# Kernel optimization log

Hardware: AMD Instinct MI355X
Metric: run time of the kernel (lower is better)

Reference implementation:

```python
import jax, jax.numpy as jnp
import numpy as np

N, E, G = 100000, 600000, 64  # nodes, edges, graphs
F_IN, W, EPS = 32, 128, 1e-5


def setup_inputs() -> dict:
    key = jax.random.key(0)
    ks = jax.random.split(key, 16)
    p = lambda k, shape: jax.random.normal(k, shape, dtype=jnp.float32) * 0.1
    z = lambda n: jnp.zeros((n,), jnp.float32)
    o = lambda n: jnp.ones((n,), jnp.float32)
    return {
        "x": jax.random.normal(ks[0], (N, F_IN), dtype=jnp.float32),
        "edge_index": jax.random.randint(ks[1], (2, E), 0, N, dtype=jnp.int32),
        "batch": jnp.sort(jax.random.randint(ks[2], (N,), 0, G, dtype=jnp.int32)),
        # GCNConv layers
        "W1": p(ks[3], (F_IN, W)), "b1": z(W),
        "W2": p(ks[4], (W, W)), "b2": z(W),
        # mlp_first: Linear -> BN -> ReLU -> Linear
        "W3": p(ks[5], (W, W)), "b3": z(W), "g1": o(W), "be1": z(W),
        "W4": p(ks[6], (W, W)), "b4": z(W),
        # mlp: Linear -> BN -> ReLU -> Linear
        "W5": p(ks[7], (W, W // 2)), "b5": z(W // 2), "g2": o(W // 2), "be2": z(W // 2),
        "W6": p(ks[8], (W // 2, 1)), "b6": z(1),
    }


def gcn_conv(x, src, dst, Wt, b):
    # PyG GCNConv with add_self_loops=True: D^-1/2 (A+I) D^-1/2 (x W) + b
    h = x @ Wt  # [N, width]
    deg = jax.ops.segment_sum(jnp.ones(src.shape[0], x.dtype), dst, num_segments=N) + 1.0
    dinv = jax.lax.rsqrt(deg)
    norm = dinv[src] * dinv[dst]  # per-edge normalization
    agg = jax.ops.segment_sum(h[src] * norm[:, None], dst, num_segments=N)
    # self-loop term: norm for (i,i) is 1/deg[i]
    return agg + h * (dinv * dinv)[:, None] + b


def batch_norm(x, g, b):
    # training-mode BatchNorm1d (batch stats, biased var)
    mu = x.mean(axis=0)
    var = jnp.mean((x - mu) ** 2, axis=0)
    return (x - mu) * jax.lax.rsqrt(var + EPS) * g + b


def reference(x, edge_index, batch, W1, b1, W2, b2, W3, b3, g1, be1, W4, b4, W5, b5, g2, be2, W6, b6):
    src, dst = edge_index[0], edge_index[1]
    x = jax.nn.relu(gcn_conv(x, src, dst, W1, b1))
    x = jax.nn.relu(gcn_conv(x, src, dst, W2, b2))
    # mlp_first + ReLU
    x = jax.nn.relu(batch_norm(x @ W3 + b3, g1, be1)) @ W4 + b4
    x = jax.nn.relu(x)
    # global max pool over nodes per graph
    x = jax.ops.segment_max(x, batch, num_segments=G)  # [G, width]
    # final mlp
    x = jax.nn.relu(batch_norm(x @ W5 + b5, g2, be2)) @ W6 + b6
    return x[:, 0]
```

## Files before the change

### kernel.cpp

```cpp
#include <hip/hip_runtime.h>

#define N_NODES 100000
#define N_EDGES 600000
#define N_GRAPHS 64
#define EPS 1e-5f
#define SCAN_BLOCKS 391

typedef unsigned short u16;
typedef unsigned int u32;
typedef __attribute__((ext_vector_type(8))) short bf16x8;
typedef __attribute__((ext_vector_type(4))) float f32x4;

__device__ __forceinline__ float bf2f(u16 u) { return __uint_as_float(((u32)u) << 16); }
__device__ __forceinline__ u16 f2bf(float f) {
    u32 u = __float_as_uint(f);
    u += 0x7FFFu + ((u >> 16) & 1u);
    return (u16)(u >> 16);
}
__device__ __forceinline__ float2 bfx2(u32 v) {
    float2 r;
    r.x = __uint_as_float(v << 16);
    r.y = __uint_as_float(v & 0xFFFF0000u);
    return r;
}

#define WS_COUNTS   ((size_t)0)
#define WS_CURSOR   ((size_t)400384)
#define WS_POOLED   ((size_t)800768)
#define WS_BNSUM    ((size_t)833536)
#define WS_BNSUMSQ  ((size_t)834048)
#define WS_FLAG     ((size_t)834560)
#define ZERO_BYTES  ((size_t)835072)
#define WS_OFFSETS  ((size_t)835072)
#define WS_DINV     ((size_t)1235456)
#define WS_DINV2    ((size_t)1635840)
#define WS_SRCS     ((size_t)2036224)
#define WS_ZF       ((size_t)4436736)
#define WS_CANONW   ((size_t)4453120)
#define WS_BUFA     ((size_t)4578560)
#define WS_BUFB     ((size_t)30178560)

#define CW_W1 0
#define CW_B1 4096
#define CW_W2 4224
#define CW_B2 20608
#define CW_W3 20736
#define CW_B3 37120
#define CW_G1 37248
#define CW_BE1 37376
#define CW_W4 37504
#define CW_B4 53888
#define CW_W5 54016
#define CW_B5 62208
#define CW_G2 62272
#define CW_BE2 62336
#define CW_W6 62400
#define CW_B6 62464

__global__ void detect_kernel(const u32* __restrict__ xraw, int* __restrict__ flag) {
    __shared__ int cnt;
    if (threadIdx.x == 0) cnt = 0;
    __syncthreads();
    int c = 0;
    for (int i = threadIdx.x; i < 2048; i += 256) {
        u32 w = xraw[i];
        float a = fabsf(__uint_as_float((w & 0xFFFFu) << 16));
        if (a == 0.f || (a > 1e-8f && a < 1e4f)) c++;
    }
    atomicAdd(&cnt, c);
    __syncthreads();
    if (threadIdx.x == 0) *flag = (cnt > 1024) ? 1 : 0;
}

__global__ void convx_kernel(const void* __restrict__ xsrc, u16* __restrict__ dst,
                             const int* __restrict__ flag, const float* __restrict__ dinv) {
    int i = blockIdx.x * 256 + threadIdx.x;
    if (i < N_NODES * 32) {
        float v = (*flag) ? bf2f(((const u16*)xsrc)[i]) : ((const float*)xsrc)[i];
        dst[i] = f2bf(v * dinv[i >> 5]);
    }
}

struct SmallArgs {
    const void* src[16];
    int n[16];
    int off[16];
    int cols[16];
};
__global__ void convs_kernel(SmallArgs a, u16* __restrict__ dst, const int* __restrict__ flag) {
    int i = blockIdx.x * 256 + threadIdx.x;
    int isbf = *flag;
#pragma unroll
    for (int j = 0; j < 16; j++)
        if (i < a.n[j]) {
            u16 v = isbf ? ((const u16*)a.src[j])[i] : f2bf(((const float*)a.src[j])[i]);
            if (a.cols[j] > 0) {
                int k = i / a.cols[j];
                int n = i - k * a.cols[j];
                int Kd = a.n[j] / a.cols[j];
                dst[a.off[j] + n * Kd + k] = v;
            } else {
                dst[a.off[j] + i] = v;
            }
        }
}

__global__ void deg_kernel(const int* __restrict__ dst, int* __restrict__ counts) {
    int e = blockIdx.x * 256 + threadIdx.x;
    if (e < N_EDGES) atomicAdd(&counts[dst[e]], 1);
}

__global__ __launch_bounds__(256) void reduce_kernel(const int* __restrict__ counts,
                                                     int* __restrict__ partials) {
    int i = blockIdx.x * 256 + threadIdx.x;
    int v = (i < N_NODES) ? counts[i] : 0;
    for (int off = 32; off > 0; off >>= 1) v += __shfl_down(v, off, 64);
    __shared__ int wsum[4];
    if ((threadIdx.x & 63) == 0) wsum[threadIdx.x >> 6] = v;
    __syncthreads();
    if (threadIdx.x == 0) partials[blockIdx.x] = wsum[0] + wsum[1] + wsum[2] + wsum[3];
}

__global__ __launch_bounds__(512) void scanpart_kernel(int* __restrict__ partials) {
    __shared__ int sc[512];
    int t = threadIdx.x;
    int v = (t < SCAN_BLOCKS) ? partials[t] : 0;
    sc[t] = v;
    __syncthreads();
    for (int off = 1; off < 512; off <<= 1) {
        int u = (t >= off) ? sc[t - off] : 0;
        __syncthreads();
        sc[t] += u;
        __syncthreads();
    }
    if (t < SCAN_BLOCKS) partials[t] = sc[t] - v;
}

__global__ __launch_bounds__(256) void offsets_kernel(const int* __restrict__ counts,
                                                      const int* __restrict__ partials,
                                                      int* __restrict__ offs,
                                                      float* __restrict__ dinv) {
    int i = blockIdx.x * 256 + threadIdx.x;
    int lane = threadIdx.x & 63, wv = threadIdx.x >> 6;
    int v = (i < N_NODES) ? counts[i] : 0;
    int sv = v;
    for (int off = 1; off < 64; off <<= 1) {
        int u = __shfl_up(sv, off, 64);
        if (lane >= off) sv += u;
    }
    __shared__ int wsum[4];
    if (lane == 63) wsum[wv] = sv;
    __syncthreads();
    int wpre = 0;
    for (int w = 0; w < wv; w++) wpre += wsum[w];
    int excl = sv - v + wpre + partials[blockIdx.x];
    if (i < N_NODES) {
        offs[i] = excl;
        dinv[i] = rsqrtf((float)(v + 1));
    }
    if (i == N_NODES - 1) offs[N_NODES] = excl + v;
}

__global__ void scatter_kernel(const int* __restrict__ src, const int* __restrict__ dst,
                               const int* __restrict__ offs, int* __restrict__ cursor,
                               int* __restrict__ srcs) {
    int e = blockIdx.x * 256 + threadIdx.x;
    if (e < N_EDGES) {
        int d = dst[e];
        int p = offs[d] + atomicAdd(&cursor[d], 1);
        srcs[p] = src[e];
    }
}

__global__ __launch_bounds__(256, 3) void gemmx_kernel(
    const u16* __restrict__ xs, const u16* __restrict__ W1t, const u16* __restrict__ b1,
    const u16* __restrict__ W2t, u16* __restrict__ C, const float* __restrict__ dinv,
    const int* __restrict__ goffs, const int* __restrict__ gsrcs, int M) {
    __shared__ __align__(16) u16 ldsA[128 * 40];
    __shared__ __align__(16) u16 ldsB[128 * 136];

    const int tid = threadIdx.x;
    const int wave = tid >> 6;
    const int lane = tid & 63;
    const int l15 = lane & 15;
    const int quad = lane >> 4;
    const int row0 = blockIdx.x * 128 + wave * 32;

    {
        const u32* g = (const u32*)W1t;
        u32* l = (u32*)ldsA;
        for (int i = tid; i < 128 * 16; i += 256) {
            int n = i >> 4, j = i & 15;
            l[n * 20 + j] = g[i];
        }
    }
    {
        const u32* g = (const u32*)W2t;
        u32* l = (u32*)ldsB;
        for (int i = tid; i < 128 * 64; i += 256) {
            int n = i >> 6, j = i & 63;
            l[n * 68 + j] = g[i];
        }
    }

    uint4 gr1[2];
#pragma unroll
    for (int rt = 0; rt < 2; rt++) {
        int r = min(row0 + rt * 16 + l15, M - 1);
        int e0 = goffs[r], e1 = goffs[r + 1];
        float ga[8];
#pragma unroll
        for (int j = 0; j < 8; j++) ga[j] = 0.f;
        const u16* Aq = xs + quad * 8;
        for (int e = e0; e < e1; e++) {
            int s = gsrcs[e];
            uint4 raw = *(const uint4*)(Aq + (size_t)s * 32);
            u32 w4[4] = {raw.x, raw.y, raw.z, raw.w};
#pragma unroll
            for (int t = 0; t < 4; t++) {
                float2 f = bfx2(w4[t]);
                ga[2 * t] += f.x;
                ga[2 * t + 1] += f.y;
            }
        }
        float di = dinv[r];
        uint4 own = *(const uint4*)(xs + (size_t)r * 32 + quad * 8);
        u32 ow[4] = {own.x, own.y, own.z, own.w};
        u32 pk[4];
#pragma unroll
        for (int t = 0; t < 4; t++) {
            float2 fo = bfx2(ow[t]);
            float vx = (ga[2 * t] + fo.x) * di;
            float vy = (ga[2 * t + 1] + fo.y) * di;
            pk[t] = (u32)f2bf(vx) | ((u32)f2bf(vy) << 16);
        }
        gr1[rt] = {pk[0], pk[1], pk[2], pk[3]};
    }
    __syncthreads();

    f32x4 acc1[2][8];
#pragma unroll
    for (int rt = 0; rt < 2; rt++)
#pragma unroll
        for (int nt = 0; nt < 8; nt++) acc1[rt][nt] = {0.f, 0.f, 0.f, 0.f};
#pragma unroll
    for (int nt = 0; nt < 8; nt++) {
        bf16x8 bf = *(const bf16x8*)&ldsA[(nt * 16 + l15) * 40 + quad * 8];
        acc1[0][nt] = __builtin_amdgcn_mfma_f32_16x16x32_bf16(
            __builtin_bit_cast(bf16x8, gr1[0]), bf, acc1[0][nt], 0, 0, 0);
        acc1[1][nt] = __builtin_amdgcn_mfma_f32_16x16x32_bf16(
            __builtin_bit_cast(bf16x8, gr1[1]), bf, acc1[1][nt], 0, 0, 0);
    }
    __syncthreads();

    float bcol[8];
#pragma unroll
    for (int nt = 0; nt < 8; nt++) bcol[nt] = bf2f(b1[nt * 16 + l15]);
    u16* tb = ldsA + wave * 1280;
    uint4 gr2[2][4];
#pragma unroll
    for (int kt = 0; kt < 4; kt++) {
#pragma unroll
        for (int rt = 0; rt < 2; rt++)
#pragma unroll
            for (int c2 = 0; c2 < 2; c2++) {
                int nt = 2 * kt + c2;
#pragma unroll
                for (int i = 0; i < 4; i++) {
                    float v = fmaxf(acc1[rt][nt][i] + bcol[nt], 0.f);
                    tb[(rt * 16 + quad * 4 + i) * 40 + c2 * 16 + l15] = f2bf(v);
                }
            }
#pragma unroll
        for (int rt = 0; rt < 2; rt++)
            gr2[rt][kt] = *(const uint4*)&tb[(rt * 16 + l15) * 40 + quad * 8];
    }

    f32x4 acc2[2][8];
#pragma unroll
    for (int rt = 0; rt < 2; rt++)
#pragma unroll
        for (int nt = 0; nt < 8; nt++) acc2[rt][nt] = {0.f, 0.f, 0.f, 0.f};
#pragma unroll
    for (int kt = 0; kt < 4; kt++) {
#pragma unroll
        for (int nt = 0; nt < 8; nt++) {
            bf16x8 bf = *(const bf16x8*)&ldsB[(nt * 16 + l15) * 136 + kt * 32 + quad * 8];
            acc2[0][nt] = __builtin_amdgcn_mfma_f32_16x16x32_bf16(
                __builtin_bit_cast(bf16x8, gr2[0][kt]), bf, acc2[0][nt], 0, 0, 0);
            acc2[1][nt] = __builtin_amdgcn_mfma_f32_16x16x32_bf16(
                __builtin_bit_cast(bf16x8, gr2[1][kt]), bf, acc2[1][nt], 0, 0, 0);
        }
    }

#pragma unroll
    for (int rt = 0; rt < 2; rt++)
#pragma unroll
        for (int i = 0; i < 4; i++) {
            int r = row0 + rt * 16 + quad * 4 + i;
            if (r < M) {
                float ds = dinv[r];
                u16* cp = C + (size_t)r * 128 + l15;
#pragma unroll
                for (int nt = 0; nt < 8; nt++) cp[nt * 16] = f2bf(acc2[rt][nt][i] * ds);
            }
        }
}

template <int K, int IN_MODE, int OUT_MODE>
__global__ __launch_bounds__(256, 3) void mgemm_kernel(
    const u16* __restrict__ A, const u16* __restrict__ Wt, const u16* __restrict__ bias,
    u16* __restrict__ C, const float* __restrict__ scl, const float* __restrict__ shf,
    const float* __restrict__ dscale, float* __restrict__ bn_sum,
    float* __restrict__ bn_sumsq, const int* __restrict__ batch, u32* __restrict__ pooled,
    const int* __restrict__ goffs, const int* __restrict__ gsrcs,
    const float* __restrict__ gdinv, const u16* __restrict__ gbias, int M) {
    constexpr int KP = K + 8;
    constexpr int NKT = K / 32;
    __shared__ __align__(16) u16 Wl[128 * KP];
    __shared__ float csum[128], csumsq[128];

    const int tid = threadIdx.x;
    const int wave = tid >> 6;
    const int lane = tid & 63;
    const int l15 = lane & 15;
    const int quad = lane >> 4;
    const int row0 = blockIdx.x * 128 + wave * 32;

    {
        const u32* g = (const u32*)Wt;
        u32* l = (u32*)Wl;
        for (int i = tid; i < 128 * (K / 2); i += 256) {
            int n = i / (K / 2), j = i - n * (K / 2);
            l[n * (KP / 2) + j] = g[i];
        }
    }
    if (OUT_MODE == 1 && tid < 128) { csum[tid] = 0.f; csumsq[tid] = 0.f; }

    uint4 gr[2][NKT];
    if (IN_MODE == 2) {
#pragma unroll
        for (int rt = 0; rt < 2; rt++) {
            int r = min(row0 + rt * 16 + l15, M - 1);
            int e0 = goffs[r], e1 = goffs[r + 1];
            float ga[NKT][8];
#pragma unroll
            for (int kt = 0; kt < NKT; kt++)
#pragma unroll
                for (int j = 0; j < 8; j++) ga[kt][j] = 0.f;
            for (int e = e0; e < e1; e++) {
                int s = gsrcs[e];
                const u16* hp = A + (size_t)s * K + quad * 8;
#pragma unroll
                for (int kt = 0; kt < NKT; kt++) {
                    uint4 raw = *(const uint4*)(hp + kt * 32);
                    u32 w4[4] = {raw.x, raw.y, raw.z, raw.w};
#pragma unroll
                    for (int t = 0; t < 4; t++) {
                        float2 f = bfx2(w4[t]);
                        ga[kt][2 * t] += f.x;
                        ga[kt][2 * t + 1] += f.y;
                    }
                }
            }
            float di = gdinv[r];
            const u16* op = A + (size_t)r * K + quad * 8;
#pragma unroll
            for (int kt = 0; kt < NKT; kt++) {
                uint4 own = *(const uint4*)(op + kt * 32);
                uint4 bb = *(const uint4*)(gbias + kt * 32 + quad * 8);
                u32 ow[4] = {own.x, own.y, own.z, own.w};
                u32 bw[4] = {bb.x, bb.y, bb.z, bb.w};
                u32 pk[4];
#pragma unroll
                for (int t = 0; t < 4; t++) {
                    float2 fo = bfx2(ow[t]);
                    float2 fb = bfx2(bw[t]);
                    float vx = fmaxf(fmaf(ga[kt][2 * t] + fo.x, di, fb.x), 0.f);
                    float vy = fmaxf(fmaf(ga[kt][2 * t + 1] + fo.y, di, fb.y), 0.f);
                    pk[t] = (u32)f2bf(vx) | ((u32)f2bf(vy) << 16);
                }
                gr[rt][kt] = {pk[0], pk[1], pk[2], pk[3]};
            }
        }
    }
    __syncthreads();

    f32x4 acc[2][8];
#pragma unroll
    for (int rt = 0; rt < 2; rt++)
#pragma unroll
        for (int nt = 0; nt < 8; nt++) acc[rt][nt] = {0.f, 0.f, 0.f, 0.f};

#pragma unroll
    for (int k0 = 0; k0 < K; k0 += 32) {
        bf16x8 af[2];
        if (IN_MODE == 2) {
#pragma unroll
            for (int rt = 0; rt < 2; rt++) af[rt] = __builtin_bit_cast(bf16x8, gr[rt][k0 / 32]);
        } else if (IN_MODE == 0) {
#pragma unroll
            for (int rt = 0; rt < 2; rt++) {
                int r = min(row0 + rt * 16 + l15, M - 1);
                af[rt] = *(const bf16x8*)(A + (size_t)r * K + k0 + quad * 8);
            }
        } else {
            float s8[8], h8[8];
#pragma unroll
            for (int t = 0; t < 8; t++) {
                s8[t] = scl[k0 + quad * 8 + t];
                h8[t] = shf[k0 + quad * 8 + t];
            }
#pragma unroll
            for (int rt = 0; rt < 2; rt++) {
                int r = min(row0 + rt * 16 + l15, M - 1);
                uint4 raw = *(const uint4*)(A + (size_t)r * K + k0 + quad * 8);
                u32 w4[4] = {raw.x, raw.y, raw.z, raw.w};
                bf16x8 tmp;
#pragma unroll
                for (int t = 0; t < 4; t++) {
                    float2 f = bfx2(w4[t]);
                    f.x = fmaxf(fmaf(f.x, s8[2 * t], h8[2 * t]), 0.f);
                    f.y = fmaxf(fmaf(f.y, s8[2 * t + 1], h8[2 * t + 1]), 0.f);
                    tmp[2 * t] = (short)f2bf(f.x);
                    tmp[2 * t + 1] = (short)f2bf(f.y);
                }
                af[rt] = tmp;
            }
        }
#pragma unroll
        for (int nt = 0; nt < 8; nt++) {
            bf16x8 bf = *(const bf16x8*)&Wl[(nt * 16 + l15) * KP + k0 + quad * 8];
            acc[0][nt] = __builtin_amdgcn_mfma_f32_16x16x32_bf16(af[0], bf, acc[0][nt], 0, 0, 0);
            acc[1][nt] = __builtin_amdgcn_mfma_f32_16x16x32_bf16(af[1], bf, acc[1][nt], 0, 0, 0);
        }
    }

    if (OUT_MODE == 0) {
#pragma unroll
        for (int rt = 0; rt < 2; rt++)
#pragma unroll
            for (int i = 0; i < 4; i++) {
                int r = row0 + rt * 16 + quad * 4 + i;
                if (r < M) {
                    float ds = dscale[r];
                    u16* cp = C + (size_t)r * 128 + l15;
#pragma unroll
                    for (int nt = 0; nt < 8; nt++) cp[nt * 16] = f2bf(acc[rt][nt][i] * ds);
                }
            }
    } else if (OUT_MODE == 1) {
        float b[8], s[8], sq[8];
#pragma unroll
        for (int nt = 0; nt < 8; nt++) {
            b[nt] = bf2f(bias[nt * 16 + l15]);
            s[nt] = 0.f;
            sq[nt] = 0.f;
        }
#pragma unroll
        for (int rt = 0; rt < 2; rt++)
#pragma unroll
            for (int i = 0; i < 4; i++) {
                int r = row0 + rt * 16 + quad * 4 + i;
                if (r < M) {
                    u16* cp = C + (size_t)r * 128 + l15;
#pragma unroll
                    for (int nt = 0; nt < 8; nt++) {
                        float v = acc[rt][nt][i] + b[nt];
                        s[nt] += v;
                        sq[nt] += v * v;
                        cp[nt * 16] = f2bf(v);
                    }
                }
            }
#pragma unroll
        for (int nt = 0; nt < 8; nt++) {
            atomicAdd(&csum[nt * 16 + l15], s[nt]);
            atomicAdd(&csumsq[nt * 16 + l15], sq[nt]);
        }
        __syncthreads();
        if (tid < 128) {
            atomicAdd(&bn_sum[tid], csum[tid]);
            atomicAdd(&bn_sumsq[tid], csumsq[tid]);
        }
    } else {
        float b[8];
#pragma unroll
        for (int nt = 0; nt < 8; nt++) b[nt] = bf2f(bias[nt * 16 + l15]);
        float cur[8];
#pragma unroll
        for (int nt = 0; nt < 8; nt++) cur[nt] = 0.f;
        int curg = -1;
#pragma unroll
        for (int rt = 0; rt < 2; rt++)
#pragma unroll
            for (int i = 0; i < 4; i++) {
                int r = row0 + rt * 16 + quad * 4 + i;
                if (r < M) {
                    int g = batch[r];
                    if (g != curg) {
                        if (curg >= 0) {
                            u32* bp = pooled + curg * 128 + l15;
#pragma unroll
                            for (int nt = 0; nt < 8; nt++)
                                if (cur[nt] > 0.f)
                                    atomicMax(&bp[nt * 16], __float_as_uint(cur[nt]));
                        }
                        curg = g;
#pragma unroll
                        for (int nt = 0; nt < 8; nt++) cur[nt] = 0.f;
                    }
#pragma unroll
                    for (int nt = 0; nt < 8; nt++)
                        cur[nt] = fmaxf(cur[nt], fmaxf(acc[rt][nt][i] + b[nt], 0.f));
                }
            }
        if (curg >= 0) {
            u32* bp = pooled + curg * 128 + l15;
#pragma unroll
            for (int nt = 0; nt < 8; nt++)
                if (cur[nt] > 0.f) atomicMax(&bp[nt * 16], __float_as_uint(cur[nt]));
        }
    }
}

__global__ void bnstats_kernel(float* __restrict__ bn_sum, float* __restrict__ bn_sumsq,
                               const u16* __restrict__ g1, const u16* __restrict__ be1) {
    int c = threadIdx.x;
    if (c < 128) {
        float mu = bn_sum[c] / (float)N_NODES;
        float var = bn_sumsq[c] / (float)N_NODES - mu * mu;
        float rstd = rsqrtf(var + EPS);
        float sc = rstd * bf2f(g1[c]);
        bn_sum[c] = sc;
        bn_sumsq[c] = bf2f(be1[c]) - mu * sc;
    }
}

__global__ __launch_bounds__(256) void head1_kernel(const u32* __restrict__ pooled,
                                                    const u16* __restrict__ W5,
                                                    const u16* __restrict__ b5,
                                                    float* __restrict__ zf) {
    __shared__ float red[4][64];
    int g = blockIdx.x;
    int c = threadIdx.x & 63;
    int kq = threadIdx.x >> 6;
    const u32* prow = pooled + g * 128;
    float p = 0.f;
    for (int k = kq * 32; k < kq * 32 + 32; k++)
        p = fmaf(__uint_as_float(prow[k]), bf2f(W5[k * 64 + c]), p);
    red[kq][c] = p;
    __syncthreads();
    if (kq == 0) zf[g * 64 + c] = red[0][c] + red[1][c] + red[2][c] + red[3][c] + bf2f(b5[c]);
}

__global__ __launch_bounds__(64) void head2_kernel(const float* __restrict__ zf,
                                                   const u16* __restrict__ g2,
                                                   const u16* __restrict__ be2,
                                                   const u16* __restrict__ W6,
                                                   const u16* __restrict__ b6,
                                                   void* __restrict__ outv,
                                                   const int* __restrict__ flag) {
    __shared__ float Z[64][65];
    __shared__ float sc[64], sh[64], w6[64];
    int t = threadIdx.x;
    for (int idx = t; idx < 4096; idx += 64) Z[idx >> 6][idx & 63] = zf[idx];
    w6[t] = bf2f(W6[t]);
    __syncthreads();
    {
        float s = 0.f, sq = 0.f;
        for (int g = 0; g < 64; g++) {
            float v = Z[g][t];
            s += v;
            sq += v * v;
        }
        float mu = s * (1.f / 64.f);
        float var = sq * (1.f / 64.f) - mu * mu;
        float rstd = rsqrtf(var + EPS);
        float scale = rstd * bf2f(g2[t]);
        sc[t] = scale;
        sh[t] = bf2f(be2[t]) - mu * scale;
    }
    __syncthreads();
    float o = 0.f;
    for (int c = 0; c < 64; c++)
        o = fmaf(fmaxf(fmaf(Z[t][c], sc[c], sh[c]), 0.f), w6[c], o);
    float res = o + bf2f(b6[0]);
    if (*flag)
        ((u16*)outv)[t] = f2bf(res);
    else
        ((float*)outv)[t] = res;
}

extern "C" void kernel_launch(void* const* d_in, const int* in_sizes, int n_in, void* d_out,
                              int out_size, void* d_ws, size_t ws_size, hipStream_t stream) {
    const void* x = d_in[0];
    const int* ei = (const int*)d_in[1];
    const int* bat = (const int*)d_in[2];

    char* ws = (char*)d_ws;
    int* counts = (int*)(ws + WS_COUNTS);
    int* cursor = (int*)(ws + WS_CURSOR);
    u32* pooled = (u32*)(ws + WS_POOLED);
    float* bnsum = (float*)(ws + WS_BNSUM);
    float* bnssq = (float*)(ws + WS_BNSUMSQ);
    int* flag = (int*)(ws + WS_FLAG);
    int* offs = (int*)(ws + WS_OFFSETS);
    float* dinv = (float*)(ws + WS_DINV);
    int* partials = (int*)(ws + WS_DINV2);
    int* srcs = (int*)(ws + WS_SRCS);
    float* zf = (float*)(ws + WS_ZF);
    u16* cw = (u16*)(ws + WS_CANONW);
    u16* bufA = (u16*)(ws + WS_BUFA);
    u16* bufB = (u16*)(ws + WS_BUFB);
    u16* xsb = bufB;

    const int* esrc = ei;
    const int* edst = ei + N_EDGES;

    hipMemsetAsync(ws, 0, ZERO_BYTES, stream);
    detect_kernel<<<1, 256, 0, stream>>>((const u32*)x, flag);

    SmallArgs sa;
    const int cw_off[16] = {CW_W1, CW_B1, CW_W2, CW_B2, CW_W3, CW_B3, CW_G1, CW_BE1,
                            CW_W4, CW_B4, CW_W5, CW_B5, CW_G2, CW_BE2, CW_W6, CW_B6};
    const int cw_n[16] = {4096, 128, 16384, 128, 16384, 128, 128, 128,
                          16384, 128, 8192, 64, 64, 64, 64, 1};
    const int cw_c[16] = {128, 0, 128, 0, 128, 0, 0, 0, 128, 0, 0, 0, 0, 0, 0, 0};
    for (int j = 0; j < 16; j++) {
        sa.src[j] = d_in[3 + j];
        sa.n[j] = cw_n[j];
        sa.off[j] = cw_off[j];
        sa.cols[j] = cw_c[j];
    }
    convs_kernel<<<64, 256, 0, stream>>>(sa, cw, flag);

    deg_kernel<<<(N_EDGES + 255) / 256, 256, 0, stream>>>(edst, counts);
    reduce_kernel<<<SCAN_BLOCKS, 256, 0, stream>>>(counts, partials);
    scanpart_kernel<<<1, 512, 0, stream>>>(partials);
    offsets_kernel<<<SCAN_BLOCKS, 256, 0, stream>>>(counts, partials, offs, dinv);
    scatter_kernel<<<(N_EDGES + 255) / 256, 256, 0, stream>>>(esrc, edst, offs, cursor, srcs);
    convx_kernel<<<(N_NODES * 32 + 255) / 256, 256, 0, stream>>>(x, xsb, flag, dinv);

    const int gb = (N_NODES + 127) / 128;
    gemmx_kernel<<<gb, 256, 0, stream>>>(xsb, cw + CW_W1, cw + CW_B1, cw + CW_W2, bufA, dinv,
                                         offs, srcs, N_NODES);
    mgemm_kernel<128, 2, 1><<<gb, 256, 0, stream>>>(bufA, cw + CW_W3, cw + CW_B3, bufB, nullptr,
                                                    nullptr, nullptr, bnsum, bnssq, nullptr,
                                                    nullptr, offs, srcs, dinv, cw + CW_B2,
                                                    N_NODES);
    bnstats_kernel<<<1, 128, 0, stream>>>(bnsum, bnssq, cw + CW_G1, cw + CW_BE1);
    mgemm_kernel<128, 1, 2><<<gb, 256, 0, stream>>>(bufB, cw + CW_W4, cw + CW_B4, nullptr, bnsum,
                                                    bnssq, nullptr, nullptr, nullptr, bat,
                                                    pooled, nullptr, nullptr, nullptr, nullptr,
                                                    N_NODES);
    head1_kernel<<<N_GRAPHS, 256, 0, stream>>>(pooled, cw + CW_W5, cw + CW_B5, zf);
    head2_kernel<<<1, 64, 0, stream>>>(zf, cw + CW_G2, cw + CW_BE2, cw + CW_W6, cw + CW_B6,
                                       d_out, flag);
}
```

Baseline: 353.0 us.

## Split neighbor aggregation into column-sliced gather kernels separate from GEMMs

Neighbor aggregation moves out of the fused GEMM kernels into standalone agg1/agg2 kernels. Features are stored in column-partitioned slabs (4 slabs of 8 for the input, 8 slabs of 16 for the hidden layer), so each gather pass touches a smaller working set and is more likely to hit in cache. The gathers also run at higher occupancy than they did inside the MFMA kernels. The cost is extra kernel launches and extra intermediate writes and reads to global memory. The first MLP GEMM now reads and writes the same buffer in place.

```diff
diff --git a/kernel.cpp b/kernel.cpp
--- a/kernel.cpp
+++ b/kernel.cpp
@@ -76,8 +76,9 @@
                              const int* __restrict__ flag, const float* __restrict__ dinv) {
     int i = blockIdx.x * 256 + threadIdx.x;
     if (i < N_NODES * 32) {
+        int r = i >> 5, c = i & 31;
         float v = (*flag) ? bf2f(((const u16*)xsrc)[i]) : ((const float*)xsrc)[i];
-        dst[i] = f2bf(v * dinv[i >> 5]);
+        dst[(size_t)(c >> 3) * (N_NODES * 8) + (size_t)r * 8 + (c & 7)] = f2bf(v * dinv[r]);
     }
 }
 
@@ -172,10 +173,100 @@
     }
 }
 
+__global__ __launch_bounds__(256, 8) void agg1_kernel(const u16* __restrict__ xs4,
+                                                      const int* __restrict__ offs,
+                                                      const int* __restrict__ srcs,
+                                                      const float* __restrict__ dinv,
+                                                      u16* __restrict__ axs) {
+    const int p = blockIdx.x & 3;
+    const int r = (blockIdx.x >> 2) * 256 + threadIdx.x;
+    if (r >= N_NODES) return;
+    const u16* base = xs4 + (size_t)p * (N_NODES * 8);
+    float acc[8];
+    {
+        uint4 own = *(const uint4*)(base + (size_t)r * 8);
+        u32 w4[4] = {own.x, own.y, own.z, own.w};
+#pragma unroll
+        for (int t = 0; t < 4; t++) {
+            float2 f = bfx2(w4[t]);
+            acc[2 * t] = f.x;
+            acc[2 * t + 1] = f.y;
+        }
+    }
+    const int e0 = offs[r], e1 = offs[r + 1];
+    for (int e = e0; e < e1; e++) {
+        int s = srcs[e];
+        uint4 raw = *(const uint4*)(base + (size_t)s * 8);
+        u32 w4[4] = {raw.x, raw.y, raw.z, raw.w};
+#pragma unroll
+        for (int t = 0; t < 4; t++) {
+            float2 f = bfx2(w4[t]);
+            acc[2 * t] += f.x;
+            acc[2 * t + 1] += f.y;
+        }
+    }
+    const float di = dinv[r];
+    uint4 outv;
+    u32* pk = (u32*)&outv;
+#pragma unroll
+    for (int t = 0; t < 4; t++)
+        pk[t] = (u32)f2bf(acc[2 * t] * di) | ((u32)f2bf(acc[2 * t + 1] * di) << 16);
+    *(uint4*)(axs + (size_t)r * 32 + p * 8) = outv;
+}
+
+__global__ __launch_bounds__(256, 8) void agg2_kernel(const u16* __restrict__ P2,
+                                                      const int* __restrict__ offs,
+                                                      const int* __restrict__ srcs,
+                                                      const float* __restrict__ dinv,
+                                                      const u16* __restrict__ b2,
+                                                      u16* __restrict__ x2) {
+    const int p = blockIdx.x & 7;
+    const int t = threadIdx.x;
+    const int r = (blockIdx.x >> 3) * 128 + (t >> 1);
+    const int half = t & 1;
+    if (r >= N_NODES) return;
+    const u16* base = P2 + (size_t)p * (N_NODES * 16) + half * 8;
+    float acc[8];
+    {
+        uint4 own = *(const uint4*)(base + (size_t)r * 16);
+        u32 w4[4] = {own.x, own.y, own.z, own.w};
+#pragma unroll
+        for (int j = 0; j < 4; j++) {
+            float2 f = bfx2(w4[j]);
+            acc[2 * j] = f.x;
+            acc[2 * j + 1] = f.y;
+        }
+    }
+    const int e0 = offs[r], e1 = offs[r + 1];
+    for (int e = e0; e < e1; e++) {
+        int s = srcs[e];
+        uint4 raw = *(const uint4*)(base + (size_t)s * 16);
+        u32 w4[4] = {raw.x, raw.y, raw.z, raw.w};
+#pragma unroll
+        for (int j = 0; j < 4; j++) {
+            float2 f = bfx2(w4[j]);
+            acc[2 * j] += f.x;
+            acc[2 * j + 1] += f.y;
+        }
+    }
+    const float di = dinv[r];
+    uint4 bb = *(const uint4*)(b2 + p * 16 + half * 8);
+    u32 bw[4] = {bb.x, bb.y, bb.z, bb.w};
+    uint4 outv;
+    u32* pk = (u32*)&outv;
+#pragma unroll
+    for (int j = 0; j < 4; j++) {
+        float2 fb = bfx2(bw[j]);
+        float vx = fmaxf(fmaf(acc[2 * j], di, fb.x), 0.f);
+        float vy = fmaxf(fmaf(acc[2 * j + 1], di, fb.y), 0.f);
+        pk[j] = (u32)f2bf(vx) | ((u32)f2bf(vy) << 16);
+    }
+    *(uint4*)(x2 + (size_t)r * 128 + p * 16 + half * 8) = outv;
+}
+
 __global__ __launch_bounds__(256, 3) void gemmx_kernel(
-    const u16* __restrict__ xs, const u16* __restrict__ W1t, const u16* __restrict__ b1,
-    const u16* __restrict__ W2t, u16* __restrict__ C, const float* __restrict__ dinv,
-    const int* __restrict__ goffs, const int* __restrict__ gsrcs, int M) {
+    const u16* __restrict__ axs, const u16* __restrict__ W1t, const u16* __restrict__ b1,
+    const u16* __restrict__ W2t, u16* __restrict__ P2, const float* __restrict__ dinv, int M) {
     __shared__ __align__(16) u16 ldsA[128 * 40];
     __shared__ __align__(16) u16 ldsB[128 * 136];
 
@@ -207,34 +298,7 @@
 #pragma unroll
     for (int rt = 0; rt < 2; rt++) {
         int r = min(row0 + rt * 16 + l15, M - 1);
-        int e0 = goffs[r], e1 = goffs[r + 1];
-        float ga[8];
-#pragma unroll
-        for (int j = 0; j < 8; j++) ga[j] = 0.f;
-        const u16* Aq = xs + quad * 8;
-        for (int e = e0; e < e1; e++) {
-            int s = gsrcs[e];
-            uint4 raw = *(const uint4*)(Aq + (size_t)s * 32);
-            u32 w4[4] = {raw.x, raw.y, raw.z, raw.w};
-#pragma unroll
-            for (int t = 0; t < 4; t++) {
-                float2 f = bfx2(w4[t]);
-                ga[2 * t] += f.x;
-                ga[2 * t + 1] += f.y;
-            }
-        }
-        float di = dinv[r];
-        uint4 own = *(const uint4*)(xs + (size_t)r * 32 + quad * 8);
-        u32 ow[4] = {own.x, own.y, own.z, own.w};
-        u32 pk[4];
-#pragma unroll
-        for (int t = 0; t < 4; t++) {
-            float2 fo = bfx2(ow[t]);
-            float vx = (ga[2 * t] + fo.x) * di;
-            float vy = (ga[2 * t + 1] + fo.y) * di;
-            pk[t] = (u32)f2bf(vx) | ((u32)f2bf(vy) << 16);
-        }
-        gr1[rt] = {pk[0], pk[1], pk[2], pk[3]};
+        gr1[rt] = *(const uint4*)(axs + (size_t)r * 32 + quad * 8);
     }
     __syncthreads();
 
@@ -300,9 +364,10 @@
             int r = row0 + rt * 16 + quad * 4 + i;
             if (r < M) {
                 float ds = dinv[r];
-                u16* cp = C + (size_t)r * 128 + l15;
-#pragma unroll
-                for (int nt = 0; nt < 8; nt++) cp[nt * 16] = f2bf(acc2[rt][nt][i] * ds);
+#pragma unroll
+                for (int nt = 0; nt < 8; nt++)
+                    P2[(size_t)nt * (N_NODES * 16) + (size_t)r * 16 + l15] =
+                        f2bf(acc2[rt][nt][i] * ds);
             }
         }
 }
@@ -311,12 +376,9 @@
 __global__ __launch_bounds__(256, 3) void mgemm_kernel(
     const u16* __restrict__ A, const u16* __restrict__ Wt, const u16* __restrict__ bias,
     u16* __restrict__ C, const float* __restrict__ scl, const float* __restrict__ shf,
-    const float* __restrict__ dscale, float* __restrict__ bn_sum,
-    float* __restrict__ bn_sumsq, const int* __restrict__ batch, u32* __restrict__ pooled,
-    const int* __restrict__ goffs, const int* __restrict__ gsrcs,
-    const float* __restrict__ gdinv, const u16* __restrict__ gbias, int M) {
+    float* __restrict__ bn_sum, float* __restrict__ bn_sumsq, const int* __restrict__ batch,
+    u32* __restrict__ pooled, int M) {
     constexpr int KP = K + 8;
-    constexpr int NKT = K / 32;
     __shared__ __align__(16) u16 Wl[128 * KP];
     __shared__ float csum[128], csumsq[128];
 
@@ -336,54 +398,6 @@
         }
     }
     if (OUT_MODE == 1 && tid < 128) { csum[tid] = 0.f; csumsq[tid] = 0.f; }
-
-    uint4 gr[2][NKT];
-    if (IN_MODE == 2) {
-#pragma unroll
-        for (int rt = 0; rt < 2; rt++) {
-            int r = min(row0 + rt * 16 + l15, M - 1);
-            int e0 = goffs[r], e1 = goffs[r + 1];
-            float ga[NKT][8];
-#pragma unroll
-            for (int kt = 0; kt < NKT; kt++)
-#pragma unroll
-                for (int j = 0; j < 8; j++) ga[kt][j] = 0.f;
-            for (int e = e0; e < e1; e++) {
-                int s = gsrcs[e];
-                const u16* hp = A + (size_t)s * K + quad * 8;
-#pragma unroll
-                for (int kt = 0; kt < NKT; kt++) {
-                    uint4 raw = *(const uint4*)(hp + kt * 32);
-                    u32 w4[4] = {raw.x, raw.y, raw.z, raw.w};
-#pragma unroll
-                    for (int t = 0; t < 4; t++) {
-                        float2 f = bfx2(w4[t]);
-                        ga[kt][2 * t] += f.x;
-                        ga[kt][2 * t + 1] += f.y;
-                    }
-                }
-            }
-            float di = gdinv[r];
-            const u16* op = A + (size_t)r * K + quad * 8;
-#pragma unroll
-            for (int kt = 0; kt < NKT; kt++) {
-                uint4 own = *(const uint4*)(op + kt * 32);
-                uint4 bb = *(const uint4*)(gbias + kt * 32 + quad * 8);
-                u32 ow[4] = {own.x, own.y, own.z, own.w};
-                u32 bw[4] = {bb.x, bb.y, bb.z, bb.w};
-                u32 pk[4];
-#pragma unroll
-                for (int t = 0; t < 4; t++) {
-                    float2 fo = bfx2(ow[t]);
-                    float2 fb = bfx2(bw[t]);
-                    float vx = fmaxf(fmaf(ga[kt][2 * t] + fo.x, di, fb.x), 0.f);
-                    float vy = fmaxf(fmaf(ga[kt][2 * t + 1] + fo.y, di, fb.y), 0.f);
-                    pk[t] = (u32)f2bf(vx) | ((u32)f2bf(vy) << 16);
-                }
-                gr[rt][kt] = {pk[0], pk[1], pk[2], pk[3]};
-            }
-        }
-    }
     __syncthreads();
 
     f32x4 acc[2][8];
@@ -395,10 +409,7 @@
 #pragma unroll
     for (int k0 = 0; k0 < K; k0 += 32) {
         bf16x8 af[2];
-        if (IN_MODE == 2) {
-#pragma unroll
-            for (int rt = 0; rt < 2; rt++) af[rt] = __builtin_bit_cast(bf16x8, gr[rt][k0 / 32]);
-        } else if (IN_MODE == 0) {
+        if (IN_MODE == 0) {
 #pragma unroll
             for (int rt = 0; rt < 2; rt++) {
                 int r = min(row0 + rt * 16 + l15, M - 1);
@@ -436,20 +447,7 @@
         }
     }
 
-    if (OUT_MODE == 0) {
-#pragma unroll
-        for (int rt = 0; rt < 2; rt++)
-#pragma unroll
-            for (int i = 0; i < 4; i++) {
-                int r = row0 + rt * 16 + quad * 4 + i;
-                if (r < M) {
-                    float ds = dscale[r];
-                    u16* cp = C + (size_t)r * 128 + l15;
-#pragma unroll
-                    for (int nt = 0; nt < 8; nt++) cp[nt * 16] = f2bf(acc[rt][nt][i] * ds);
-                }
-            }
-    } else if (OUT_MODE == 1) {
+    if (OUT_MODE == 1) {
         float b[8], s[8], sq[8];
 #pragma unroll
         for (int nt = 0; nt < 8; nt++) {
@@ -611,9 +609,10 @@
     int* srcs = (int*)(ws + WS_SRCS);
     float* zf = (float*)(ws + WS_ZF);
     u16* cw = (u16*)(ws + WS_CANONW);
-    u16* bufA = (u16*)(ws + WS_BUFA);
-    u16* bufB = (u16*)(ws + WS_BUFB);
-    u16* xsb = bufB;
+    u16* P2 = (u16*)(ws + WS_BUFA);
+    u16* xs4 = (u16*)(ws + WS_BUFB);
+    u16* axs = (u16*)(ws + WS_BUFB) + 3200000;
+    u16* x2 = (u16*)(ws + WS_BUFB);
 
     const int* esrc = ei;
     const int* edst = ei + N_EDGES;
@@ -640,19 +639,19 @@
     scanpart_kernel<<<1, 512, 0, stream>>>(partials);
     offsets_kernel<<<SCAN_BLOCKS, 256, 0, stream>>>(counts, partials, offs, dinv);
     scatter_kernel<<<(N_EDGES + 255) / 256, 256, 0, stream>>>(esrc, edst, offs, cursor, srcs);
-    convx_kernel<<<(N_NODES * 32 + 255) / 256, 256, 0, stream>>>(x, xsb, flag, dinv);
+    convx_kernel<<<(N_NODES * 32 + 255) / 256, 256, 0, stream>>>(x, xs4, flag, dinv);
 
     const int gb = (N_NODES + 127) / 128;
-    gemmx_kernel<<<gb, 256, 0, stream>>>(xsb, cw + CW_W1, cw + CW_B1, cw + CW_W2, bufA, dinv,
-                                         offs, srcs, N_NODES);
-    mgemm_kernel<128, 2, 1><<<gb, 256, 0, stream>>>(bufA, cw + CW_W3, cw + CW_B3, bufB, nullptr,
-                                                    nullptr, nullptr, bnsum, bnssq, nullptr,
-                                                    nullptr, offs, srcs, dinv, cw + CW_B2,
+    agg1_kernel<<<4 * SCAN_BLOCKS, 256, 0, stream>>>(xs4, offs, srcs, dinv, axs);
+    gemmx_kernel<<<gb, 256, 0, stream>>>(axs, cw + CW_W1, cw + CW_B1, cw + CW_W2, P2, dinv,
+                                         N_NODES);
+    agg2_kernel<<<8 * gb, 256, 0, stream>>>(P2, offs, srcs, dinv, cw + CW_B2, x2);
+    mgemm_kernel<128, 0, 1><<<gb, 256, 0, stream>>>(x2, cw + CW_W3, cw + CW_B3, x2, nullptr,
+                                                    nullptr, bnsum, bnssq, nullptr, nullptr,
                                                     N_NODES);
     bnstats_kernel<<<1, 128, 0, stream>>>(bnsum, bnssq, cw + CW_G1, cw + CW_BE1);
-    mgemm_kernel<128, 1, 2><<<gb, 256, 0, stream>>>(bufB, cw + CW_W4, cw + CW_B4, nullptr, bnsum,
-                                                    bnssq, nullptr, nullptr, nullptr, bat,
-                                                    pooled, nullptr, nullptr, nullptr, nullptr,
+    mgemm_kernel<128, 1, 2><<<gb, 256, 0, stream>>>(x2, cw + CW_W4, cw + CW_B4, nullptr, bnsum,
+                                                    bnssq, nullptr, nullptr, bat, pooled,
                                                     N_NODES);
     head1_kernel<<<N_GRAPHS, 256, 0, stream>>>(pooled, cw + CW_W5, cw + CW_B5, zf);
     head2_kernel<<<1, 64, 0, stream>>>(zf, cw + CW_G2, cw + CW_BE2, cw + CW_W6, cw + CW_B6,
```

New measurement: 367.9 us. +4.2%, slower.
